# Kernel optimization log

Measured on AMD Instinct MI355X. Metric: run time of the kernel, lower is better.

## Reference

```python
import jax, jax.numpy as jnp
import numpy as np

B, T, D, H = 8, 1024, 1024, 16
DH = D // H  # head dim = 64


def setup_inputs() -> dict:
    key = jax.random.key(0)
    ks = jax.random.split(key, 16)
    std_qk = np.sqrt(2.0 / (D + DH)).astype(np.float32)
    inp = {
        "query": jax.random.normal(ks[0], (B, T, D), jnp.float32),
        "key": jax.random.normal(ks[1], (B, T, D), jnp.float32),
        "value": jax.random.normal(ks[2], (B, T, D), jnp.float32),
        "spatial_encoding": jax.random.normal(ks[3], (B, T, T), jnp.float32),
        "edge_encoding": jax.random.normal(ks[4], (B, T, T), jnp.float32),
        "key_padding_mask": jax.random.bernoulli(ks[5], 0.1, (B, T)),  # True = masked key
        # Linear params stored as (in, out); y = x @ W + b (equivalent to torch x @ W.T + b)
        "Wq": jax.random.normal(ks[6], (D, D), jnp.float32) * std_qk,
        "bq": jnp.zeros((D,), jnp.float32),
        "Wk": jax.random.normal(ks[7], (D, D), jnp.float32) * std_qk,
        "bk": jnp.zeros((D,), jnp.float32),
        "Wv": jax.random.normal(ks[8], (D, D), jnp.float32) * std_qk,
        "bv": jnp.zeros((D,), jnp.float32),
        "Wo": jax.random.normal(ks[9], (D, D), jnp.float32),
        "bo": jnp.zeros((D,), jnp.float32),
    }
    return inp


def reference(query, key, value, spatial_encoding, edge_encoding, key_padding_mask,
              Wq, bq, Wk, bk, Wv, bv, Wo, bo):
    # QKV projections -> (B, H, T, DH)
    def proj(x, W, b):
        return (x @ W + b).reshape(B, T, H, DH).transpose(0, 2, 1, 3)

    q = proj(query, Wq, bq)
    k = proj(key, Wk, bk)
    v = proj(value, Wv, bv)

    # attention bias: spatial + edge, masked by key padding (broadcast over heads)
    attn_bias = (spatial_encoding + edge_encoding)[:, None, :, :]  # (B,1,T,T)
    neg_inf = jnp.float32(-jnp.inf)
    attn_bias = jnp.where(key_padding_mask[:, None, None, :], neg_inf, attn_bias)

    scale = 1.0 / np.sqrt(DH).astype(np.float32)
    scores = jnp.einsum('bhqd,bhkd->bhqk', q, k) * scale + attn_bias  # (B,H,T,T)
    attn = jax.nn.softmax(scores, axis=-1)
    out = jnp.einsum('bhqk,bhkd->bhqd', attn, v)  # (B,H,T,DH)
    out = out.transpose(0, 2, 1, 3).reshape(B, T, D)
    return out @ Wo + bo
```

## Files before the change

kernel.cpp:

```cpp
#include <hip/hip_runtime.h>
#include <hip/hip_bf16.h>

#define BB 8
#define TT 1024
#define DD 1024
#define HH 16
#define DH 64

typedef __attribute__((ext_vector_type(8))) short short8;
typedef __attribute__((ext_vector_type(4))) float f32x4;

__device__ __forceinline__ unsigned short f2bf(float f) {
  unsigned int u = __builtin_bit_cast(unsigned int, f);
  unsigned int rounding = 0x7fffu + ((u >> 16) & 1u);
  u += rounding;
  return (unsigned short)(u >> 16);
}
__device__ __forceinline__ float bf2f(unsigned short u) {
  unsigned int x = ((unsigned int)u) << 16;
  return __builtin_bit_cast(float, x);
}

__global__ __launch_bounds__(256) void convertT_k(const float* __restrict__ in,
                                                  unsigned short* __restrict__ out) {
  int g = blockIdx.x * 256 + threadIdx.x;
  int n = g & (DD - 1);
  int kb = (g >> 10) * 8;
  short8 o;
#pragma unroll
  for (int j = 0; j < 8; ++j)
    o[j] = (short)f2bf(in[(size_t)(kb + j) * DD + n]);
  *(short8*)(out + (size_t)n * DD + kb) = o;
}

template<int AF32, int OF32>
__global__ __launch_bounds__(256) void gemm_k(const void* __restrict__ Ap,
                                              const unsigned short* __restrict__ Wt,
                                              const float* __restrict__ bias,
                                              void* __restrict__ Cp,
                                              int M, int N, int K) {
  __shared__ unsigned short As[128][40];
  __shared__ unsigned short Bs[128][40];
  const int tid = threadIdx.x;
  const int lane = tid & 63;
  const int w = tid >> 6;
  const int lo = lane & 15, hi = lane >> 4;
  const int wm = w >> 1, wn = w & 1;
  const int m0 = blockIdx.y * 128, n0 = blockIdx.x * 128;
  f32x4 acc[4][4] = {};
  for (int k0 = 0; k0 < K; k0 += 32) {
#pragma unroll
    for (int it = 0; it < 2; ++it) {
      int c = tid + 256 * it;
      int r = c >> 2, cb = (c & 3) * 8;
      short8 sv;
      if constexpr (AF32) {
        const float* src = (const float*)Ap + (size_t)(m0 + r) * K + k0 + cb;
        float4 v0 = *(const float4*)src;
        float4 v1 = *(const float4*)(src + 4);
        sv[0] = (short)f2bf(v0.x); sv[1] = (short)f2bf(v0.y);
        sv[2] = (short)f2bf(v0.z); sv[3] = (short)f2bf(v0.w);
        sv[4] = (short)f2bf(v1.x); sv[5] = (short)f2bf(v1.y);
        sv[6] = (short)f2bf(v1.z); sv[7] = (short)f2bf(v1.w);
      } else {
        sv = *(const short8*)((const unsigned short*)Ap + (size_t)(m0 + r) * K + k0 + cb);
      }
      *(short8*)&As[r][cb] = sv;
    }
#pragma unroll
    for (int it = 0; it < 2; ++it) {
      int c = tid + 256 * it;
      int nn = c >> 2, k8 = (c & 3) * 8;
      short8 v = *(const short8*)(Wt + (size_t)(n0 + nn) * K + k0 + k8);
      *(short8*)&Bs[nn][k8] = v;
    }
    __syncthreads();
    short8 af[4], bf[4];
#pragma unroll
    for (int mt = 0; mt < 4; ++mt) af[mt] = *(const short8*)&As[wm * 64 + mt * 16 + lo][hi * 8];
#pragma unroll
    for (int nt = 0; nt < 4; ++nt) bf[nt] = *(const short8*)&Bs[wn * 64 + nt * 16 + lo][hi * 8];
#pragma unroll
    for (int mt = 0; mt < 4; ++mt)
#pragma unroll
      for (int nt = 0; nt < 4; ++nt)
        acc[mt][nt] = __builtin_amdgcn_mfma_f32_16x16x32_bf16(af[mt], bf[nt], acc[mt][nt], 0, 0, 0);
    __syncthreads();
  }
#pragma unroll
  for (int mt = 0; mt < 4; ++mt) {
#pragma unroll
    for (int nt = 0; nt < 4; ++nt) {
      int col = n0 + wn * 64 + nt * 16 + lo;
      float bv = bias[col];
#pragma unroll
      for (int r = 0; r < 4; ++r) {
        int row = m0 + wm * 64 + mt * 16 + hi * 4 + r;
        float v = acc[mt][nt][r] + bv;
        if constexpr (OF32) ((float*)Cp)[(size_t)row * N + col] = v;
        else ((unsigned short*)Cp)[(size_t)row * N + col] = f2bf(v);
      }
    }
  }
}

__global__ __launch_bounds__(256) void transpose_v_k(const unsigned short* __restrict__ Vp,
                                                     unsigned short* __restrict__ Vt) {
  __shared__ unsigned short tile[64][72];
  const int blk = blockIdx.x;
  const int t0 = (blk & 15) * 64;
  const int h = (blk >> 4) & 15;
  const int b = blk >> 8;
  const int tid = threadIdx.x;
#pragma unroll
  for (int it = 0; it < 2; ++it) {
    int c = tid + 256 * it;
    int r = c >> 3, d8 = (c & 7) * 8;
    short8 v = *(const short8*)(Vp + ((size_t)(b * TT + t0 + r)) * DD + h * DH + d8);
    *(short8*)&tile[r][d8] = v;
  }
  __syncthreads();
#pragma unroll
  for (int it = 0; it < 2; ++it) {
    int c = tid + 256 * it;
    int d = c >> 3, t8 = (c & 7) * 8;
    short8 o;
#pragma unroll
    for (int j = 0; j < 8; ++j) o[j] = (short)tile[t8 + j][d];
    *(short8*)(Vt + ((size_t)(b * HH + h) * DH + d) * TT + t0 + t8) = o;
  }
}

__global__ __launch_bounds__(256) void attn_k(const unsigned short* __restrict__ Qp,
                                              const unsigned short* __restrict__ Kp,
                                              const unsigned short* __restrict__ Vt,
                                              const float* __restrict__ spat,
                                              const float* __restrict__ edge,
                                              const int* __restrict__ mask,
                                              unsigned short* __restrict__ Obf) {
  __shared__ unsigned short P[4][16][40];
  const int blk = blockIdx.x;
  const int qt = blk & 15;
  const int h = (blk >> 4) & 15;
  const int b = blk >> 8;
  const int tid = threadIdx.x;
  const int w = tid >> 6;
  const int lane = tid & 63;
  const int lo = lane & 15, hi = lane >> 4;
  const int q0 = qt * 64 + w * 16;

  const unsigned short* Qb = Qp + ((size_t)b * TT + q0) * DD + h * DH;
  const unsigned short* Kb = Kp + ((size_t)b * TT) * DD + h * DH;
  const unsigned short* Vb = Vt + (size_t)(b * HH + h) * DH * TT;
  const float* Sp = spat + (size_t)b * TT * TT;
  const float* Ed = edge + (size_t)b * TT * TT;
  const int* Mk = mask + b * TT;

  short8 qf0 = *(const short8*)(Qb + (size_t)lo * DD + hi * 8);
  short8 qf1 = *(const short8*)(Qb + (size_t)lo * DD + 32 + hi * 8);

  float m[4], l[4];
  f32x4 acc[4] = {};
#pragma unroll
  for (int r = 0; r < 4; ++r) { m[r] = -INFINITY; l[r] = 0.f; }

  for (int k0 = 0; k0 < TT; k0 += 32) {
    short8 kf00, kf01, kf10, kf11;
    {
      const unsigned short* kp0 = Kb + (size_t)(k0 + lo) * DD + hi * 8;
      const unsigned short* kp1 = Kb + (size_t)(k0 + 16 + lo) * DD + hi * 8;
      kf00 = *(const short8*)kp0;  kf01 = *(const short8*)(kp0 + 32);
      kf10 = *(const short8*)kp1;  kf11 = *(const short8*)(kp1 + 32);
    }
    f32x4 sc0 = {}, sc1 = {};
    sc0 = __builtin_amdgcn_mfma_f32_16x16x32_bf16(qf0, kf00, sc0, 0, 0, 0);
    sc0 = __builtin_amdgcn_mfma_f32_16x16x32_bf16(qf1, kf01, sc0, 0, 0, 0);
    sc1 = __builtin_amdgcn_mfma_f32_16x16x32_bf16(qf0, kf10, sc1, 0, 0, 0);
    sc1 = __builtin_amdgcn_mfma_f32_16x16x32_bf16(qf1, kf11, sc1, 0, 0, 0);

    const int mk0 = Mk[k0 + lo];
    const int mk1 = Mk[k0 + 16 + lo];

    float p0[4], p1[4], alpha[4];
#pragma unroll
    for (int r = 0; r < 4; ++r) {
      const size_t roff = (size_t)(q0 + hi * 4 + r) * TT + k0;
      const float* srow = Sp + roff;
      const float* erow = Ed + roff;
      float b0 = mk0 ? -1e30f : (srow[lo] + erow[lo]);
      float b1 = mk1 ? -1e30f : (srow[16 + lo] + erow[16 + lo]);
      float s0 = sc0[r] * 0.125f + b0;
      float s1 = sc1[r] * 0.125f + b1;
      float mx = fmaxf(s0, s1);
      mx = fmaxf(mx, __shfl_xor(mx, 1));
      mx = fmaxf(mx, __shfl_xor(mx, 2));
      mx = fmaxf(mx, __shfl_xor(mx, 4));
      mx = fmaxf(mx, __shfl_xor(mx, 8));
      float mn = fmaxf(m[r], mx);
      alpha[r] = __expf(m[r] - mn);
      m[r] = mn;
      p0[r] = __expf(s0 - mn);
      p1[r] = __expf(s1 - mn);
      float rs = p0[r] + p1[r];
      rs += __shfl_xor(rs, 1);
      rs += __shfl_xor(rs, 2);
      rs += __shfl_xor(rs, 4);
      rs += __shfl_xor(rs, 8);
      l[r] = l[r] * alpha[r] + rs;
    }
#pragma unroll
    for (int dt = 0; dt < 4; ++dt)
#pragma unroll
      for (int r = 0; r < 4; ++r) acc[dt][r] *= alpha[r];

#pragma unroll
    for (int r = 0; r < 4; ++r) {
      P[w][hi * 4 + r][lo] = f2bf(p0[r]);
      P[w][hi * 4 + r][lo + 16] = f2bf(p1[r]);
    }
    short8 pf = *(const short8*)&P[w][lo][hi * 8];
#pragma unroll
    for (int dt = 0; dt < 4; ++dt) {
      short8 vf = *(const short8*)(Vb + (size_t)(dt * 16 + lo) * TT + k0 + hi * 8);
      acc[dt] = __builtin_amdgcn_mfma_f32_16x16x32_bf16(pf, vf, acc[dt], 0, 0, 0);
    }
  }

  unsigned short* Ob = Obf + ((size_t)b * TT + q0) * DD + h * DH;
#pragma unroll
  for (int dt = 0; dt < 4; ++dt)
#pragma unroll
    for (int r = 0; r < 4; ++r) {
      float o = acc[dt][r] / l[r];
      Ob[(size_t)(hi * 4 + r) * DD + dt * 16 + lo] = f2bf(o);
    }
}

extern "C" void kernel_launch(void* const* d_in, const int* in_sizes, int n_in,
                              void* d_out, int out_size, void* d_ws, size_t ws_size,
                              hipStream_t stream) {
  const float* query = (const float*)d_in[0];
  const float* key   = (const float*)d_in[1];
  const float* value = (const float*)d_in[2];
  const float* spat  = (const float*)d_in[3];
  const float* edge  = (const float*)d_in[4];
  const int*   maskp = (const int*)d_in[5];
  const float* Wq = (const float*)d_in[6];  const float* bq = (const float*)d_in[7];
  const float* Wk = (const float*)d_in[8];  const float* bk = (const float*)d_in[9];
  const float* Wv = (const float*)d_in[10]; const float* bv = (const float*)d_in[11];
  const float* Wo = (const float*)d_in[12]; const float* bo = (const float*)d_in[13];
  float* out = (float*)d_out;

  unsigned short* WqT = (unsigned short*)d_ws;
  unsigned short* WkT = WqT + (size_t)DD * DD;
  unsigned short* WvT = WkT + (size_t)DD * DD;
  unsigned short* WoT = WvT + (size_t)DD * DD;
  unsigned short* Qp    = WoT + (size_t)DD * DD;
  unsigned short* Kp    = Qp + (size_t)BB * TT * DD;
  unsigned short* Vp    = Kp + (size_t)BB * TT * DD;
  unsigned short* Vt    = Vp + (size_t)BB * TT * DD;
  unsigned short* Obf   = Vt + (size_t)BB * TT * DD;

  const int M = BB * TT;
  const int cvtBlocks = DD * DD / 8 / 256;

  convertT_k<<<cvtBlocks, 256, 0, stream>>>(Wq, WqT);
  convertT_k<<<cvtBlocks, 256, 0, stream>>>(Wk, WkT);
  convertT_k<<<cvtBlocks, 256, 0, stream>>>(Wv, WvT);
  convertT_k<<<cvtBlocks, 256, 0, stream>>>(Wo, WoT);

  gemm_k<1, 0><<<dim3(DD / 128, M / 128), 256, 0, stream>>>(query, WqT, bq, Qp, M, DD, DD);
  gemm_k<1, 0><<<dim3(DD / 128, M / 128), 256, 0, stream>>>(key,   WkT, bk, Kp, M, DD, DD);
  gemm_k<1, 0><<<dim3(DD / 128, M / 128), 256, 0, stream>>>(value, WvT, bv, Vp, M, DD, DD);

  transpose_v_k<<<BB * HH * (TT / 64), 256, 0, stream>>>(Vp, Vt);

  attn_k<<<BB * HH * (TT / 64), 256, 0, stream>>>(Qp, Kp, Vt, spat, edge, maskp, Obf);

  gemm_k<0, 1><<<dim3(DD / 128, M / 128), 256, 0, stream>>>(Obf, WoT, bo, out, M, DD, DD);
}
```

Measured before the change: 711.9 us.

## Fuse QKV projections and weight conversions, add direct-to-LDS GEMM loads, widen attention tile

Merges the four weight-convert launches into one and the three QKV GEMMs into a single launch writing an interleaved QKV buffer. Both GEMMs now use a K-step of 64, asynchronous global_load_lds for the bf16 operands, and an XOR-swizzled LDS layout to avoid bank conflicts. The attention loop processes 64 keys per iteration, which halves the number of online-softmax rescale steps, and the final division is replaced by a reciprocal multiply. The cost is higher register and LDS use per block, and the row stride of Q/K reads grows to 3072.

```diff
diff --git a/kernel.cpp b/kernel.cpp
--- a/kernel.cpp
+++ b/kernel.cpp
@@ -6,6 +6,7 @@
 #define DD 1024
 #define HH 16
 #define DH 64
+#define QKVLD 3072
 
 typedef __attribute__((ext_vector_type(8))) short short8;
 typedef __attribute__((ext_vector_type(4))) float f32x4;
@@ -16,95 +17,176 @@
   u += rounding;
   return (unsigned short)(u >> 16);
 }
-__device__ __forceinline__ float bf2f(unsigned short u) {
-  unsigned int x = ((unsigned int)u) << 16;
-  return __builtin_bit_cast(float, x);
-}
-
-__global__ __launch_bounds__(256) void convertT_k(const float* __restrict__ in,
-                                                  unsigned short* __restrict__ out) {
-  int g = blockIdx.x * 256 + threadIdx.x;
+
+__device__ __forceinline__ void gload16(const void* g, void* l) {
+  __builtin_amdgcn_global_load_lds((const __attribute__((address_space(1))) void*)g,
+                                   (__attribute__((address_space(3))) void*)l, 16, 0, 0);
+}
+
+__global__ __launch_bounds__(256) void convertT4_k(const float* __restrict__ w0,
+                                                   const float* __restrict__ w1,
+                                                   const float* __restrict__ w2,
+                                                   const float* __restrict__ w3,
+                                                   unsigned short* __restrict__ out) {
+  int bx = blockIdx.x;
+  int seg = bx >> 9;
+  const float* in = seg == 0 ? w0 : seg == 1 ? w1 : seg == 2 ? w2 : w3;
+  unsigned short* o = out + (size_t)seg * DD * DD;
+  int g = (bx & 511) * 256 + threadIdx.x;
   int n = g & (DD - 1);
   int kb = (g >> 10) * 8;
-  short8 o;
-#pragma unroll
-  for (int j = 0; j < 8; ++j)
-    o[j] = (short)f2bf(in[(size_t)(kb + j) * DD + n]);
-  *(short8*)(out + (size_t)n * DD + kb) = o;
-}
-
-template<int AF32, int OF32>
-__global__ __launch_bounds__(256) void gemm_k(const void* __restrict__ Ap,
-                                              const unsigned short* __restrict__ Wt,
-                                              const float* __restrict__ bias,
-                                              void* __restrict__ Cp,
-                                              int M, int N, int K) {
-  __shared__ unsigned short As[128][40];
-  __shared__ unsigned short Bs[128][40];
-  const int tid = threadIdx.x;
-  const int lane = tid & 63;
-  const int w = tid >> 6;
+  short8 v;
+#pragma unroll
+  for (int j = 0; j < 8; ++j) v[j] = (short)f2bf(in[(size_t)(kb + j) * DD + n]);
+  *(short8*)(o + (size_t)n * DD + kb) = v;
+}
+
+__global__ __launch_bounds__(256) void gemm_qkv_k(const float* __restrict__ Aq,
+                                                  const float* __restrict__ Ak,
+                                                  const float* __restrict__ Av,
+                                                  const unsigned short* __restrict__ Wt3,
+                                                  const float* __restrict__ bq,
+                                                  const float* __restrict__ bk,
+                                                  const float* __restrict__ bv,
+                                                  unsigned short* __restrict__ C) {
+  __shared__ unsigned short Bs[128 * 64];
+  __shared__ unsigned short As[128 * 72];
+  const int tid = threadIdx.x, lane = tid & 63, w = tid >> 6;
   const int lo = lane & 15, hi = lane >> 4;
   const int wm = w >> 1, wn = w & 1;
-  const int m0 = blockIdx.y * 128, n0 = blockIdx.x * 128;
+  const int seg = blockIdx.x >> 3;
+  const float* Ap = seg == 0 ? Aq : seg == 1 ? Ak : Av;
+  const float* bias = seg == 0 ? bq : seg == 1 ? bk : bv;
+  const int n0 = blockIdx.x * 128;
+  const int m0 = blockIdx.y * 128;
   f32x4 acc[4][4] = {};
-  for (int k0 = 0; k0 < K; k0 += 32) {
-#pragma unroll
-    for (int it = 0; it < 2; ++it) {
+  int dmn[4], dmk[4];
+#pragma unroll
+  for (int i = 0; i < 4; ++i) {
+    int d = i * 4096 + w * 1024 + lane * 16;
+    int lz = d ^ (((d >> 7) & 7) << 4);
+    dmn[i] = d >> 7;
+    dmk[i] = (lz & 127) >> 1;
+  }
+  for (int k0 = 0; k0 < DD; k0 += 64) {
+#pragma unroll
+    for (int i = 0; i < 4; ++i)
+      gload16(Wt3 + (size_t)(n0 + dmn[i]) * DD + k0 + dmk[i], &Bs[(i * 4096 + w * 1024) >> 1]);
+#pragma unroll
+    for (int it = 0; it < 4; ++it) {
       int c = tid + 256 * it;
-      int r = c >> 2, cb = (c & 3) * 8;
+      int r = c >> 3, cb = (c & 7) * 8;
+      const float* src = Ap + (size_t)(m0 + r) * DD + k0 + cb;
+      float4 v0 = *(const float4*)src;
+      float4 v1 = *(const float4*)(src + 4);
       short8 sv;
-      if constexpr (AF32) {
-        const float* src = (const float*)Ap + (size_t)(m0 + r) * K + k0 + cb;
-        float4 v0 = *(const float4*)src;
-        float4 v1 = *(const float4*)(src + 4);
-        sv[0] = (short)f2bf(v0.x); sv[1] = (short)f2bf(v0.y);
-        sv[2] = (short)f2bf(v0.z); sv[3] = (short)f2bf(v0.w);
-        sv[4] = (short)f2bf(v1.x); sv[5] = (short)f2bf(v1.y);
-        sv[6] = (short)f2bf(v1.z); sv[7] = (short)f2bf(v1.w);
-      } else {
-        sv = *(const short8*)((const unsigned short*)Ap + (size_t)(m0 + r) * K + k0 + cb);
-      }
-      *(short8*)&As[r][cb] = sv;
-    }
-#pragma unroll
-    for (int it = 0; it < 2; ++it) {
-      int c = tid + 256 * it;
-      int nn = c >> 2, k8 = (c & 3) * 8;
-      short8 v = *(const short8*)(Wt + (size_t)(n0 + nn) * K + k0 + k8);
-      *(short8*)&Bs[nn][k8] = v;
+      sv[0] = (short)f2bf(v0.x); sv[1] = (short)f2bf(v0.y);
+      sv[2] = (short)f2bf(v0.z); sv[3] = (short)f2bf(v0.w);
+      sv[4] = (short)f2bf(v1.x); sv[5] = (short)f2bf(v1.y);
+      sv[6] = (short)f2bf(v1.z); sv[7] = (short)f2bf(v1.w);
+      *(short8*)&As[r * 72 + cb] = sv;
     }
     __syncthreads();
-    short8 af[4], bf[4];
-#pragma unroll
-    for (int mt = 0; mt < 4; ++mt) af[mt] = *(const short8*)&As[wm * 64 + mt * 16 + lo][hi * 8];
-#pragma unroll
-    for (int nt = 0; nt < 4; ++nt) bf[nt] = *(const short8*)&Bs[wn * 64 + nt * 16 + lo][hi * 8];
-#pragma unroll
-    for (int mt = 0; mt < 4; ++mt)
-#pragma unroll
-      for (int nt = 0; nt < 4; ++nt)
-        acc[mt][nt] = __builtin_amdgcn_mfma_f32_16x16x32_bf16(af[mt], bf[nt], acc[mt][nt], 0, 0, 0);
+#pragma unroll
+    for (int s = 0; s < 2; ++s) {
+      short8 af[4], bf[4];
+#pragma unroll
+      for (int mt = 0; mt < 4; ++mt)
+        af[mt] = *(const short8*)&As[(wm * 64 + mt * 16 + lo) * 72 + s * 32 + hi * 8];
+#pragma unroll
+      for (int nt = 0; nt < 4; ++nt) {
+        int nr = wn * 64 + nt * 16 + lo;
+        int byte = (nr * 128 + s * 64 + hi * 16) ^ ((nr & 7) << 4);
+        bf[nt] = *(const short8*)((const char*)Bs + byte);
+      }
+#pragma unroll
+      for (int mt = 0; mt < 4; ++mt)
+#pragma unroll
+        for (int nt = 0; nt < 4; ++nt)
+          acc[mt][nt] = __builtin_amdgcn_mfma_f32_16x16x32_bf16(af[mt], bf[nt], acc[mt][nt], 0, 0, 0);
+    }
     __syncthreads();
   }
 #pragma unroll
-  for (int mt = 0; mt < 4; ++mt) {
+  for (int mt = 0; mt < 4; ++mt)
+#pragma unroll
+    for (int nt = 0; nt < 4; ++nt) {
+      int cl = wn * 64 + nt * 16 + lo;
+      float bvv = bias[(n0 & 1023) + cl];
+      int col = n0 + cl;
+#pragma unroll
+      for (int r = 0; r < 4; ++r) {
+        int row = m0 + wm * 64 + mt * 16 + hi * 4 + r;
+        C[(size_t)row * QKVLD + col] = f2bf(acc[mt][nt][r] + bvv);
+      }
+    }
+}
+
+__global__ __launch_bounds__(256) void gemm_out_k(const unsigned short* __restrict__ Aobf,
+                                                  const unsigned short* __restrict__ WoT,
+                                                  const float* __restrict__ bo,
+                                                  float* __restrict__ out) {
+  __shared__ unsigned short Bs[128 * 64];
+  __shared__ unsigned short As[128 * 64];
+  const int tid = threadIdx.x, lane = tid & 63, w = tid >> 6;
+  const int lo = lane & 15, hi = lane >> 4;
+  const int wm = w >> 1, wn = w & 1;
+  const int n0 = blockIdx.x * 128;
+  const int m0 = blockIdx.y * 128;
+  f32x4 acc[4][4] = {};
+  int dmn[4], dmk[4];
+#pragma unroll
+  for (int i = 0; i < 4; ++i) {
+    int d = i * 4096 + w * 1024 + lane * 16;
+    int lz = d ^ (((d >> 7) & 7) << 4);
+    dmn[i] = d >> 7;
+    dmk[i] = (lz & 127) >> 1;
+  }
+  for (int k0 = 0; k0 < DD; k0 += 64) {
+#pragma unroll
+    for (int i = 0; i < 4; ++i) {
+      gload16(WoT + (size_t)(n0 + dmn[i]) * DD + k0 + dmk[i], &Bs[(i * 4096 + w * 1024) >> 1]);
+      gload16(Aobf + (size_t)(m0 + dmn[i]) * DD + k0 + dmk[i], &As[(i * 4096 + w * 1024) >> 1]);
+    }
+    __syncthreads();
+#pragma unroll
+    for (int s = 0; s < 2; ++s) {
+      short8 af[4], bf[4];
+#pragma unroll
+      for (int mt = 0; mt < 4; ++mt) {
+        int mr = wm * 64 + mt * 16 + lo;
+        int byte = (mr * 128 + s * 64 + hi * 16) ^ ((mr & 7) << 4);
+        af[mt] = *(const short8*)((const char*)As + byte);
+      }
+#pragma unroll
+      for (int nt = 0; nt < 4; ++nt) {
+        int nr = wn * 64 + nt * 16 + lo;
+        int byte = (nr * 128 + s * 64 + hi * 16) ^ ((nr & 7) << 4);
+        bf[nt] = *(const short8*)((const char*)Bs + byte);
+      }
+#pragma unroll
+      for (int mt = 0; mt < 4; ++mt)
+#pragma unroll
+        for (int nt = 0; nt < 4; ++nt)
+          acc[mt][nt] = __builtin_amdgcn_mfma_f32_16x16x32_bf16(af[mt], bf[nt], acc[mt][nt], 0, 0, 0);
+    }
+    __syncthreads();
+  }
+#pragma unroll
+  for (int mt = 0; mt < 4; ++mt)
 #pragma unroll
     for (int nt = 0; nt < 4; ++nt) {
       int col = n0 + wn * 64 + nt * 16 + lo;
-      float bv = bias[col];
+      float bvv = bo[col];
 #pragma unroll
       for (int r = 0; r < 4; ++r) {
         int row = m0 + wm * 64 + mt * 16 + hi * 4 + r;
-        float v = acc[mt][nt][r] + bv;
-        if constexpr (OF32) ((float*)Cp)[(size_t)row * N + col] = v;
-        else ((unsigned short*)Cp)[(size_t)row * N + col] = f2bf(v);
-      }
-    }
-  }
-}
-
-__global__ __launch_bounds__(256) void transpose_v_k(const unsigned short* __restrict__ Vp,
+        out[(size_t)row * DD + col] = acc[mt][nt][r] + bvv;
+      }
+    }
+}
+
+__global__ __launch_bounds__(256) void transpose_v_k(const unsigned short* __restrict__ QKV,
                                                      unsigned short* __restrict__ Vt) {
   __shared__ unsigned short tile[64][72];
   const int blk = blockIdx.x;
@@ -116,7 +198,7 @@
   for (int it = 0; it < 2; ++it) {
     int c = tid + 256 * it;
     int r = c >> 3, d8 = (c & 7) * 8;
-    short8 v = *(const short8*)(Vp + ((size_t)(b * TT + t0 + r)) * DD + h * DH + d8);
+    short8 v = *(const short8*)(QKV + ((size_t)(b * TT + t0 + r)) * QKVLD + 2048 + h * DH + d8);
     *(short8*)&tile[r][d8] = v;
   }
   __syncthreads();
@@ -131,14 +213,13 @@
   }
 }
 
-__global__ __launch_bounds__(256) void attn_k(const unsigned short* __restrict__ Qp,
-                                              const unsigned short* __restrict__ Kp,
+__global__ __launch_bounds__(256) void attn_k(const unsigned short* __restrict__ QKV,
                                               const unsigned short* __restrict__ Vt,
                                               const float* __restrict__ spat,
                                               const float* __restrict__ edge,
                                               const int* __restrict__ mask,
                                               unsigned short* __restrict__ Obf) {
-  __shared__ unsigned short P[4][16][40];
+  __shared__ unsigned short P[4][16][72];
   const int blk = blockIdx.x;
   const int qt = blk & 15;
   const int h = (blk >> 4) & 15;
@@ -149,49 +230,54 @@
   const int lo = lane & 15, hi = lane >> 4;
   const int q0 = qt * 64 + w * 16;
 
-  const unsigned short* Qb = Qp + ((size_t)b * TT + q0) * DD + h * DH;
-  const unsigned short* Kb = Kp + ((size_t)b * TT) * DD + h * DH;
+  const unsigned short* Qb = QKV + ((size_t)(b * TT + q0)) * QKVLD + h * DH;
+  const unsigned short* Kb = QKV + (size_t)b * TT * QKVLD + 1024 + h * DH;
   const unsigned short* Vb = Vt + (size_t)(b * HH + h) * DH * TT;
   const float* Sp = spat + (size_t)b * TT * TT;
   const float* Ed = edge + (size_t)b * TT * TT;
   const int* Mk = mask + b * TT;
 
-  short8 qf0 = *(const short8*)(Qb + (size_t)lo * DD + hi * 8);
-  short8 qf1 = *(const short8*)(Qb + (size_t)lo * DD + 32 + hi * 8);
+  short8 qf0 = *(const short8*)(Qb + (size_t)lo * QKVLD + hi * 8);
+  short8 qf1 = *(const short8*)(Qb + (size_t)lo * QKVLD + 32 + hi * 8);
 
   float m[4], l[4];
   f32x4 acc[4] = {};
 #pragma unroll
   for (int r = 0; r < 4; ++r) { m[r] = -INFINITY; l[r] = 0.f; }
 
-  for (int k0 = 0; k0 < TT; k0 += 32) {
-    short8 kf00, kf01, kf10, kf11;
-    {
-      const unsigned short* kp0 = Kb + (size_t)(k0 + lo) * DD + hi * 8;
-      const unsigned short* kp1 = Kb + (size_t)(k0 + 16 + lo) * DD + hi * 8;
-      kf00 = *(const short8*)kp0;  kf01 = *(const short8*)(kp0 + 32);
-      kf10 = *(const short8*)kp1;  kf11 = *(const short8*)(kp1 + 32);
-    }
-    f32x4 sc0 = {}, sc1 = {};
-    sc0 = __builtin_amdgcn_mfma_f32_16x16x32_bf16(qf0, kf00, sc0, 0, 0, 0);
-    sc0 = __builtin_amdgcn_mfma_f32_16x16x32_bf16(qf1, kf01, sc0, 0, 0, 0);
-    sc1 = __builtin_amdgcn_mfma_f32_16x16x32_bf16(qf0, kf10, sc1, 0, 0, 0);
-    sc1 = __builtin_amdgcn_mfma_f32_16x16x32_bf16(qf1, kf11, sc1, 0, 0, 0);
-
-    const int mk0 = Mk[k0 + lo];
-    const int mk1 = Mk[k0 + 16 + lo];
-
-    float p0[4], p1[4], alpha[4];
+  for (int k0 = 0; k0 < TT; k0 += 64) {
+    short8 kf[8];
+#pragma unroll
+    for (int kt = 0; kt < 4; ++kt) {
+      const unsigned short* kp = Kb + (size_t)(k0 + kt * 16 + lo) * QKVLD + hi * 8;
+      kf[kt * 2] = *(const short8*)kp;
+      kf[kt * 2 + 1] = *(const short8*)(kp + 32);
+    }
+    int mk[4];
+#pragma unroll
+    for (int kt = 0; kt < 4; ++kt) mk[kt] = Mk[k0 + kt * 16 + lo];
+
+    f32x4 sc[4];
+#pragma unroll
+    for (int kt = 0; kt < 4; ++kt) {
+      f32x4 z = {};
+      z = __builtin_amdgcn_mfma_f32_16x16x32_bf16(qf0, kf[kt * 2], z, 0, 0, 0);
+      sc[kt] = __builtin_amdgcn_mfma_f32_16x16x32_bf16(qf1, kf[kt * 2 + 1], z, 0, 0, 0);
+    }
+
+    float alpha[4];
 #pragma unroll
     for (int r = 0; r < 4; ++r) {
       const size_t roff = (size_t)(q0 + hi * 4 + r) * TT + k0;
       const float* srow = Sp + roff;
       const float* erow = Ed + roff;
-      float b0 = mk0 ? -1e30f : (srow[lo] + erow[lo]);
-      float b1 = mk1 ? -1e30f : (srow[16 + lo] + erow[16 + lo]);
-      float s0 = sc0[r] * 0.125f + b0;
-      float s1 = sc1[r] * 0.125f + b1;
-      float mx = fmaxf(s0, s1);
+      float s[4];
+#pragma unroll
+      for (int j = 0; j < 4; ++j) {
+        float bb = mk[j] ? -1e30f : (srow[j * 16 + lo] + erow[j * 16 + lo]);
+        s[j] = sc[j][r] * 0.125f + bb;
+      }
+      float mx = fmaxf(fmaxf(s[0], s[1]), fmaxf(s[2], s[3]));
       mx = fmaxf(mx, __shfl_xor(mx, 1));
       mx = fmaxf(mx, __shfl_xor(mx, 2));
       mx = fmaxf(mx, __shfl_xor(mx, 4));
@@ -199,9 +285,13 @@
       float mn = fmaxf(m[r], mx);
       alpha[r] = __expf(m[r] - mn);
       m[r] = mn;
-      p0[r] = __expf(s0 - mn);
-      p1[r] = __expf(s1 - mn);
-      float rs = p0[r] + p1[r];
+      float rs = 0.f;
+#pragma unroll
+      for (int j = 0; j < 4; ++j) {
+        s[j] = __expf(s[j] - mn);
+        rs += s[j];
+        P[w][hi * 4 + r][j * 16 + lo] = f2bf(s[j]);
+      }
       rs += __shfl_xor(rs, 1);
       rs += __shfl_xor(rs, 2);
       rs += __shfl_xor(rs, 4);
@@ -214,26 +304,25 @@
       for (int r = 0; r < 4; ++r) acc[dt][r] *= alpha[r];
 
 #pragma unroll
-    for (int r = 0; r < 4; ++r) {
-      P[w][hi * 4 + r][lo] = f2bf(p0[r]);
-      P[w][hi * 4 + r][lo + 16] = f2bf(p1[r]);
-    }
-    short8 pf = *(const short8*)&P[w][lo][hi * 8];
-#pragma unroll
-    for (int dt = 0; dt < 4; ++dt) {
-      short8 vf = *(const short8*)(Vb + (size_t)(dt * 16 + lo) * TT + k0 + hi * 8);
-      acc[dt] = __builtin_amdgcn_mfma_f32_16x16x32_bf16(pf, vf, acc[dt], 0, 0, 0);
-    }
-  }
-
+    for (int kc = 0; kc < 2; ++kc) {
+      short8 pf = *(const short8*)&P[w][lo][kc * 32 + hi * 8];
+#pragma unroll
+      for (int dt = 0; dt < 4; ++dt) {
+        short8 vf = *(const short8*)(Vb + (size_t)(dt * 16 + lo) * TT + k0 + kc * 32 + hi * 8);
+        acc[dt] = __builtin_amdgcn_mfma_f32_16x16x32_bf16(pf, vf, acc[dt], 0, 0, 0);
+      }
+    }
+  }
+
+  float rl[4];
+#pragma unroll
+  for (int r = 0; r < 4; ++r) rl[r] = 1.0f / l[r];
   unsigned short* Ob = Obf + ((size_t)b * TT + q0) * DD + h * DH;
 #pragma unroll
   for (int dt = 0; dt < 4; ++dt)
 #pragma unroll
-    for (int r = 0; r < 4; ++r) {
-      float o = acc[dt][r] / l[r];
-      Ob[(size_t)(hi * 4 + r) * DD + dt * 16 + lo] = f2bf(o);
-    }
+    for (int r = 0; r < 4; ++r)
+      Ob[(size_t)(hi * 4 + r) * DD + dt * 16 + lo] = f2bf(acc[dt][r] * rl[r]);
 }
 
 extern "C" void kernel_launch(void* const* d_in, const int* in_sizes, int n_in,
@@ -251,31 +340,20 @@
   const float* Wo = (const float*)d_in[12]; const float* bo = (const float*)d_in[13];
   float* out = (float*)d_out;
 
-  unsigned short* WqT = (unsigned short*)d_ws;
-  unsigned short* WkT = WqT + (size_t)DD * DD;
-  unsigned short* WvT = WkT + (size_t)DD * DD;
-  unsigned short* WoT = WvT + (size_t)DD * DD;
-  unsigned short* Qp    = WoT + (size_t)DD * DD;
-  unsigned short* Kp    = Qp + (size_t)BB * TT * DD;
-  unsigned short* Vp    = Kp + (size_t)BB * TT * DD;
-  unsigned short* Vt    = Vp + (size_t)BB * TT * DD;
-  unsigned short* Obf   = Vt + (size_t)BB * TT * DD;
-
   const int M = BB * TT;
-  const int cvtBlocks = DD * DD / 8 / 256;
-
-  convertT_k<<<cvtBlocks, 256, 0, stream>>>(Wq, WqT);
-  convertT_k<<<cvtBlocks, 256, 0, stream>>>(Wk, WkT);
-  convertT_k<<<cvtBlocks, 256, 0, stream>>>(Wv, WvT);
-  convertT_k<<<cvtBlocks, 256, 0, stream>>>(Wo, WoT);
-
-  gemm_k<1, 0><<<dim3(DD / 128, M / 128), 256, 0, stream>>>(query, WqT, bq, Qp, M, DD, DD);
-  gemm_k<1, 0><<<dim3(DD / 128, M / 128), 256, 0, stream>>>(key,   WkT, bk, Kp, M, DD, DD);
-  gemm_k<1, 0><<<dim3(DD / 128, M / 128), 256, 0, stream>>>(value, WvT, bv, Vp, M, DD, DD);
-
-  transpose_v_k<<<BB * HH * (TT / 64), 256, 0, stream>>>(Vp, Vt);
-
-  attn_k<<<BB * HH * (TT / 64), 256, 0, stream>>>(Qp, Kp, Vt, spat, edge, maskp, Obf);
-
-  gemm_k<0, 1><<<dim3(DD / 128, M / 128), 256, 0, stream>>>(Obf, WoT, bo, out, M, DD, DD);
-}
+  unsigned short* WT3 = (unsigned short*)d_ws;
+  unsigned short* WoT = WT3 + (size_t)3 * DD * DD;
+  unsigned short* QKV = WoT + (size_t)DD * DD;
+  unsigned short* Vt  = QKV + (size_t)M * QKVLD;
+  unsigned short* Obf = Vt + (size_t)M * DD;
+
+  convertT4_k<<<2048, 256, 0, stream>>>(Wq, Wk, Wv, Wo, WT3);
+
+  gemm_qkv_k<<<dim3(24, M / 128), 256, 0, stream>>>(query, key, value, WT3, bq, bk, bv, QKV);
+
+  transpose_v_k<<<BB * HH * (TT / 64), 256, 0, stream>>>(QKV, Vt);
+
+  attn_k<<<BB * HH * (TT / 64), 256, 0, stream>>>(QKV, Vt, spat, edge, maskp, Obf);
+
+  gemm_out_k<<<dim3(DD / 128, M / 128), 256, 0, stream>>>(Obf, WoT, bo, out);
+}
```

Result: slower. 746.4 us (+4.9%).
